# Optimization experiments

Hardware: AMD Instinct MI355X
Metric: run time of the kernel (lower is better)

Reference implementation:

```python
import jax, jax.numpy as jnp
import numpy as np

D = 256  # input_dim
B = 2048

def setup_inputs() -> dict:
    key = jax.random.key(0)
    ks = jax.random.split(key, 6)
    x = jax.random.normal(ks[0], (B, D), dtype=jnp.float32)
    offsets = jax.random.normal(ks[1], (D,), dtype=jnp.float32)
    coeff0 = jax.random.normal(ks[2], (), dtype=jnp.float32)
    coeff1 = jax.random.normal(ks[3], (D,), dtype=jnp.float32)
    coeff2 = jax.random.normal(ks[4], (D, D), dtype=jnp.float32)
    coeff3 = jax.random.normal(ks[5], (D, D, D), dtype=jnp.float32)
    return {"x": x, "offsets": offsets, "coeff0": coeff0, "coeff1": coeff1,
            "coeff2": coeff2, "coeff3": coeff3}

def reference(x, offsets, coeff0, coeff1, coeff2, coeff3):
    # Truncated Taylor series around learned offsets: out[b] = c0 + sum_i <coeff_i, rel^{\otimes i}>[b]
    rel = x - offsets  # (B, D)
    out = coeff0  # scalar, broadcasts to (B,)
    for c in (coeff1, coeff2, coeff3):
        # contract one mode of the rank-i coefficient with rel at a time
        t = jnp.einsum('...d,bd->b...', c, rel)  # (B, D^{i-1})
        while t.ndim > 1:
            t = jnp.einsum('b...d,bd->b...', t, rel)
        out = out + t  # (B,)
    return out
```

## Files before the change

### kernel.cpp

```cpp
#include <hip/hip_runtime.h>
#include <hip/hip_bf16.h>

#define DD 256
#define BB 2048
#define BM 128
#define BN 64
#define NTILE ((DD * DD) / BM)
#define NSTAGE (BB / BN)

typedef __bf16 bf16x8 __attribute__((ext_vector_type(8)));
typedef float  f32x4  __attribute__((ext_vector_type(4)));

#define AS1 __attribute__((address_space(1)))
#define AS3 __attribute__((address_space(3)))

__device__ __forceinline__ unsigned short f2bf(float f) {
    unsigned int u = __float_as_uint(f);
    return (unsigned short)((u + 0x7FFFu + ((u >> 16) & 1u)) >> 16);
}
__device__ __forceinline__ float bf2f(unsigned short s) {
    return __uint_as_float(((unsigned int)s) << 16);
}
__device__ __forceinline__ void async_cp16(const void* g, void* l) {
    __builtin_amdgcn_global_load_lds((const AS1 unsigned int*)g,
                                     (AS3 unsigned int*)l, 16, 0, 0);
}

__global__ void prep_all(const float* __restrict__ x, const float* __restrict__ offsets,
                         const float* __restrict__ c0, const float* __restrict__ c1,
                         float* __restrict__ rel_f32, unsigned short* __restrict__ rel_bf16,
                         float* __restrict__ out) {
    const int tid = threadIdx.x, wave = tid >> 6, lane = tid & 63;
    const float4 o4  = *(const float4*)(offsets + lane * 4);
    const float4 c14 = *(const float4*)(c1 + lane * 4);
#pragma unroll
    for (int i = 0; i < 2; ++i) {
        const int b = blockIdx.x * 8 + wave * 2 + i;
        const float4 x4 = *(const float4*)(x + (size_t)b * DD + lane * 4);
        float4 r;
        r.x = x4.x - o4.x; r.y = x4.y - o4.y; r.z = x4.z - o4.z; r.w = x4.w - o4.w;
        *(float4*)(rel_f32 + (size_t)b * DD + lane * 4) = r;
        ushort4 rb;
        rb.x = f2bf(r.x); rb.y = f2bf(r.y); rb.z = f2bf(r.z); rb.w = f2bf(r.w);
        *(ushort4*)(rel_bf16 + (size_t)b * DD + lane * 4) = rb;
        float s = r.x * c14.x + r.y * c14.y + r.z * c14.z + r.w * c14.w;
        s += __shfl_xor(s, 1);  s += __shfl_xor(s, 2);  s += __shfl_xor(s, 4);
        s += __shfl_xor(s, 8);  s += __shfl_xor(s, 16); s += __shfl_xor(s, 32);
        if (lane == 0) out[b] = c0[0] + s;
    }
}

__global__ __launch_bounds__(256, 2) void taylor3(
    const float* __restrict__ c3, const float* __restrict__ c2,
    const float* __restrict__ rel_f32, const unsigned short* __restrict__ rel_bf16,
    float* __restrict__ partial)
{
    __shared__ unsigned short Bs[2][BN * DD];
    __shared__ float relI[BB];
    __shared__ float c2row[BM];
    __shared__ float colsum[2][4][BN];

    const int tile = blockIdx.x;
    const int i_t   = tile >> 1;
    const int jbase = (tile & 1) << 7;
    const int tid  = threadIdx.x;
    const int wave = tid >> 6;
    const int lane = tid & 63;
    const int wm = wave & 1, wk = wave >> 1;
    const int lrow = lane & 15, quad = lane >> 4;

#pragma unroll
    for (int k = 0; k < 8; ++k) {
        const int b = tid + k * 256;
        relI[b] = rel_f32[(size_t)b * DD + i_t];
    }
    if (tid < BM) c2row[tid] = c2[i_t * DD + jbase + tid];

    bf16x8 afr[4][4];
    {
        const float* abase = c3 + (size_t)tile * BM * DD;
#pragma unroll
        for (int mt = 0; mt < 4; ++mt) {
            const int row = wm * 64 + mt * 16 + lrow;
            const float* p = abase + (size_t)row * DD + wk * 128 + quad * 8;
#pragma unroll
            for (int ks = 0; ks < 4; ++ks) {
                float4 f0 = *(const float4*)(p + ks * 32);
                float4 f1 = *(const float4*)(p + ks * 32 + 4);
                union { unsigned short u[8]; bf16x8 v; } cv;
                cv.u[0] = f2bf(f0.x); cv.u[1] = f2bf(f0.y);
                cv.u[2] = f2bf(f0.z); cv.u[3] = f2bf(f0.w);
                cv.u[4] = f2bf(f1.x); cv.u[5] = f2bf(f1.y);
                cv.u[6] = f2bf(f1.z); cv.u[7] = f2bf(f1.w);
                afr[ks][mt] = cv.v;
            }
        }
    }

    auto stage = [&](int nb, int buf) {
        const int b0 = nb * BN;
#pragma unroll
        for (int c = 0; c < 8; ++c) {
            const int r0 = c * 8 + wave * 2;
            const int row = r0 + (lane >> 5);
            const int g = (lane & 31) ^ (row & 7);
            const unsigned short* src = rel_bf16 + (size_t)(b0 + row) * DD + g * 8;
            async_cp16(src, &Bs[buf][r0 * DD]);
        }
    };

    stage(0, 0);
    int prev_b0 = -1;

    for (int nb = 0; nb < NSTAGE; ++nb) {
        const int cur = nb & 1;
        const int b0 = nb * BN;
        __syncthreads();
        if (nb + 1 < NSTAGE) stage(nb + 1, cur ^ 1);

        if (prev_b0 >= 0 && tid < BN) {
            const float v = colsum[cur ^ 1][0][tid] + colsum[cur ^ 1][1][tid]
                          + colsum[cur ^ 1][2][tid] + colsum[cur ^ 1][3][tid];
            partial[(size_t)tile * BB + prev_b0 + tid] = relI[prev_b0 + tid] * v;
        }

        f32x4 acc[4][4];
#pragma unroll
        for (int mt = 0; mt < 4; ++mt)
#pragma unroll
            for (int nt = 0; nt < 4; ++nt)
                acc[mt][nt] = (f32x4){0.f, 0.f, 0.f, 0.f};

#pragma unroll
        for (int ks = 0; ks < 4; ++ks) {
            const int glog = wk * 16 + ks * 4 + quad;
            bf16x8 bfr[4];
#pragma unroll
            for (int nt = 0; nt < 4; ++nt) {
                const int col = nt * 16 + lrow;
                const int g = glog ^ (col & 7);
                bfr[nt] = *(const bf16x8*)(&Bs[cur][col * DD + g * 8]);
            }
#pragma unroll
            for (int mt = 0; mt < 4; ++mt)
#pragma unroll
                for (int nt = 0; nt < 4; ++nt)
                    acc[mt][nt] = __builtin_amdgcn_mfma_f32_16x16x32_bf16(
                        afr[ks][mt], bfr[nt], acc[mt][nt], 0, 0, 0);
        }

        float sv[4];
#pragma unroll
        for (int nt = 0; nt < 4; ++nt) {
            const int col = nt * 16 + lrow;
            float s = 0.f;
#pragma unroll
            for (int mt = 0; mt < 4; ++mt) {
                const int el = wm * 64 + mt * 16 + quad * 4;
                const int e  = jbase + el;
                const int g  = (e >> 3) ^ (col & 7);
                const ushort4 rj = *(const ushort4*)(&Bs[cur][col * DD + g * 8 + (e & 7)]);
                float c2x = 0.f, c2y = 0.f, c2z = 0.f, c2w = 0.f;
                if (wk == 0) {
                    const float4 c2r = *(const float4*)(&c2row[el]);
                    c2x = c2r.x; c2y = c2r.y; c2z = c2r.z; c2w = c2r.w;
                }
                s += (acc[mt][nt][0] + c2x) * bf2f(rj.x);
                s += (acc[mt][nt][1] + c2y) * bf2f(rj.y);
                s += (acc[mt][nt][2] + c2z) * bf2f(rj.z);
                s += (acc[mt][nt][3] + c2w) * bf2f(rj.w);
            }
            s += __shfl_xor(s, 16, 64);
            s += __shfl_xor(s, 32, 64);
            sv[nt] = s;
        }
        {
            const float v01 = (quad & 1) ? sv[1] : sv[0];
            const float v23 = (quad & 1) ? sv[3] : sv[2];
            colsum[cur][wave][lane] = (quad & 2) ? v23 : v01;
        }
        prev_b0 = b0;
    }
    __syncthreads();
    if (tid < BN) {
        const float v = colsum[1][0][tid] + colsum[1][1][tid]
                      + colsum[1][2][tid] + colsum[1][3][tid];
        partial[(size_t)tile * BB + prev_b0 + tid] = relI[prev_b0 + tid] * v;
    }
}

__global__ void reduce_partial(const float* __restrict__ partial, float* __restrict__ out) {
    __shared__ f32x4 red[256];
    const int t = threadIdx.x;
    const int g = blockIdx.x * 4 + (t & 3);
    const int slice = t >> 2;
    f32x4 s = (f32x4){0.f, 0.f, 0.f, 0.f};
    for (int r = slice * 8; r < slice * 8 + 8; ++r)
        s += *(const f32x4*)(partial + (size_t)r * BB + g * 4);
    red[t] = s; __syncthreads();
    if (t < 128) red[t] += red[t + 128]; __syncthreads();
    if (t < 64)  red[t] += red[t + 64];  __syncthreads();
    if (t < 32)  red[t] += red[t + 32];  __syncthreads();
    if (t < 16)  red[t] += red[t + 16];  __syncthreads();
    if (t < 8)   red[t] += red[t + 8];   __syncthreads();
    if (t < 4) {
        const f32x4 v = red[t] + red[t + 4];
        float4* op = (float4*)(out + (size_t)(blockIdx.x * 4 + t) * 4);
        float4 o = *op;
        o.x += v[0]; o.y += v[1]; o.z += v[2]; o.w += v[3];
        *op = o;
    }
}

extern "C" void kernel_launch(void* const* d_in, const int* in_sizes, int n_in,
                              void* d_out, int out_size, void* d_ws, size_t ws_size,
                              hipStream_t stream) {
    const float* x       = (const float*)d_in[0];
    const float* offsets = (const float*)d_in[1];
    const float* c0      = (const float*)d_in[2];
    const float* c1      = (const float*)d_in[3];
    const float* c2      = (const float*)d_in[4];
    const float* c3      = (const float*)d_in[5];
    float* out = (float*)d_out;

    char* ws = (char*)d_ws;
    float* rel_f32 = (float*)ws;
    unsigned short* rel_bf16 = (unsigned short*)(ws + (size_t)BB * DD * 4);
    float* partial = (float*)(ws + (size_t)BB * DD * 6);

    prep_all<<<BB / 8, 256, 0, stream>>>(x, offsets, c0, c1, rel_f32, rel_bf16, out);
    taylor3<<<NTILE, 256, 0, stream>>>(c3, c2, rel_f32, rel_bf16, partial);
    reduce_partial<<<128, 256, 0, stream>>>(partial, out);
}
```

Measured before the change: 188.6 us.

## Split K dimension across blocks to double grid and raise occupancy

```diff
diff --git a/kernel.cpp b/kernel.cpp
--- a/kernel.cpp
+++ b/kernel.cpp
@@ -4,8 +4,8 @@
 #define DD 256
 #define BB 2048
 #define BM 128
-#define BN 64
-#define NTILE ((DD * DD) / BM)
+#define BN 32
+#define NBLK 1024
 #define NSTAGE (BB / BN)
 
 typedef __bf16 bf16x8 __attribute__((ext_vector_type(8)));
@@ -26,41 +26,32 @@
                                      (AS3 unsigned int*)l, 16, 0, 0);
 }
 
-__global__ void prep_all(const float* __restrict__ x, const float* __restrict__ offsets,
-                         const float* __restrict__ c0, const float* __restrict__ c1,
-                         float* __restrict__ rel_f32, unsigned short* __restrict__ rel_bf16,
-                         float* __restrict__ out) {
-    const int tid = threadIdx.x, wave = tid >> 6, lane = tid & 63;
-    const float4 o4  = *(const float4*)(offsets + lane * 4);
-    const float4 c14 = *(const float4*)(c1 + lane * 4);
-#pragma unroll
-    for (int i = 0; i < 2; ++i) {
-        const int b = blockIdx.x * 8 + wave * 2 + i;
-        const float4 x4 = *(const float4*)(x + (size_t)b * DD + lane * 4);
-        float4 r;
-        r.x = x4.x - o4.x; r.y = x4.y - o4.y; r.z = x4.z - o4.z; r.w = x4.w - o4.w;
-        *(float4*)(rel_f32 + (size_t)b * DD + lane * 4) = r;
-        ushort4 rb;
-        rb.x = f2bf(r.x); rb.y = f2bf(r.y); rb.z = f2bf(r.z); rb.w = f2bf(r.w);
-        *(ushort4*)(rel_bf16 + (size_t)b * DD + lane * 4) = rb;
-        float s = r.x * c14.x + r.y * c14.y + r.z * c14.z + r.w * c14.w;
-        s += __shfl_xor(s, 1);  s += __shfl_xor(s, 2);  s += __shfl_xor(s, 4);
-        s += __shfl_xor(s, 8);  s += __shfl_xor(s, 16); s += __shfl_xor(s, 32);
-        if (lane == 0) out[b] = c0[0] + s;
-    }
-}
-
-__global__ __launch_bounds__(256, 2) void taylor3(
+__global__ void prep_rel(const float* __restrict__ x, const float* __restrict__ offsets,
+                         float* __restrict__ rel_f32, unsigned short* __restrict__ rel_bf16) {
+    const int fi = blockIdx.x * 256 + threadIdx.x;
+    const int d4 = fi & 63;
+    const float4 o4 = ((const float4*)offsets)[d4];
+    const float4 x4 = ((const float4*)x)[fi];
+    float4 r;
+    r.x = x4.x - o4.x; r.y = x4.y - o4.y; r.z = x4.z - o4.z; r.w = x4.w - o4.w;
+    ((float4*)rel_f32)[fi] = r;
+    ushort4 rb;
+    rb.x = f2bf(r.x); rb.y = f2bf(r.y); rb.z = f2bf(r.z); rb.w = f2bf(r.w);
+    ((ushort4*)rel_bf16)[fi] = rb;
+}
+
+__global__ __launch_bounds__(256, 4) void taylor3(
     const float* __restrict__ c3, const float* __restrict__ c2,
     const float* __restrict__ rel_f32, const unsigned short* __restrict__ rel_bf16,
     float* __restrict__ partial)
 {
-    __shared__ unsigned short Bs[2][BN * DD];
-    __shared__ float relI[BB];
+    __shared__ unsigned short Bs[2][BN * 128];
     __shared__ float c2row[BM];
     __shared__ float colsum[2][4][BN];
 
-    const int tile = blockIdx.x;
+    const int bid  = blockIdx.x;
+    const int tile = bid >> 1;
+    const int kh   = bid & 1;
     const int i_t   = tile >> 1;
     const int jbase = (tile & 1) << 7;
     const int tid  = threadIdx.x;
@@ -69,22 +60,18 @@
     const int wm = wave & 1, wk = wave >> 1;
     const int lrow = lane & 15, quad = lane >> 4;
 
-#pragma unroll
-    for (int k = 0; k < 8; ++k) {
-        const int b = tid + k * 256;
-        relI[b] = rel_f32[(size_t)b * DD + i_t];
-    }
     if (tid < BM) c2row[tid] = c2[i_t * DD + jbase + tid];
 
-    bf16x8 afr[4][4];
+    bf16x8 afr[2][4];
     {
         const float* abase = c3 + (size_t)tile * BM * DD;
+        const int koff = kh * 128 + wk * 64 + quad * 8;
 #pragma unroll
         for (int mt = 0; mt < 4; ++mt) {
             const int row = wm * 64 + mt * 16 + lrow;
-            const float* p = abase + (size_t)row * DD + wk * 128 + quad * 8;
-#pragma unroll
-            for (int ks = 0; ks < 4; ++ks) {
+            const float* p = abase + (size_t)row * DD + koff;
+#pragma unroll
+            for (int ks = 0; ks < 2; ++ks) {
                 float4 f0 = *(const float4*)(p + ks * 32);
                 float4 f1 = *(const float4*)(p + ks * 32 + 4);
                 union { unsigned short u[8]; bf16x8 v; } cv;
@@ -100,12 +87,12 @@
     auto stage = [&](int nb, int buf) {
         const int b0 = nb * BN;
 #pragma unroll
-        for (int c = 0; c < 8; ++c) {
-            const int r0 = c * 8 + wave * 2;
-            const int row = r0 + (lane >> 5);
-            const int g = (lane & 31) ^ (row & 7);
-            const unsigned short* src = rel_bf16 + (size_t)(b0 + row) * DD + g * 8;
-            async_cp16(src, &Bs[buf][r0 * DD]);
+        for (int c = 0; c < 2; ++c) {
+            const int r0 = c * 16 + wave * 4;
+            const int row = r0 + (lane >> 4);
+            const int gsrc = (lane & 15) ^ (row & 15);
+            const unsigned short* src = rel_bf16 + (size_t)(b0 + row) * DD + kh * 128 + gsrc * 8;
+            async_cp16(src, &Bs[buf][r0 * 128]);
         }
     };
 
@@ -121,95 +108,107 @@
         if (prev_b0 >= 0 && tid < BN) {
             const float v = colsum[cur ^ 1][0][tid] + colsum[cur ^ 1][1][tid]
                           + colsum[cur ^ 1][2][tid] + colsum[cur ^ 1][3][tid];
-            partial[(size_t)tile * BB + prev_b0 + tid] = relI[prev_b0 + tid] * v;
-        }
-
-        f32x4 acc[4][4];
+            const float relI = rel_f32[(size_t)(prev_b0 + tid) * DD + i_t];
+            partial[(size_t)bid * BB + prev_b0 + tid] = relI * v;
+        }
+
+        ushort4 rj[2][4];
+#pragma unroll
+        for (int nt = 0; nt < 2; ++nt) {
+            const int bg = b0 + nt * 16 + lrow;
+#pragma unroll
+            for (int mt = 0; mt < 4; ++mt) {
+                const int e = jbase + wm * 64 + mt * 16 + quad * 4;
+                rj[nt][mt] = *(const ushort4*)(rel_bf16 + (size_t)bg * DD + e);
+            }
+        }
+
+        f32x4 acc[4][2];
 #pragma unroll
         for (int mt = 0; mt < 4; ++mt)
 #pragma unroll
-            for (int nt = 0; nt < 4; ++nt)
+            for (int nt = 0; nt < 2; ++nt)
                 acc[mt][nt] = (f32x4){0.f, 0.f, 0.f, 0.f};
 
 #pragma unroll
-        for (int ks = 0; ks < 4; ++ks) {
-            const int glog = wk * 16 + ks * 4 + quad;
-            bf16x8 bfr[4];
-#pragma unroll
-            for (int nt = 0; nt < 4; ++nt) {
+        for (int ks = 0; ks < 2; ++ks) {
+            const int glog = wk * 8 + ks * 4 + quad;
+            bf16x8 bfr[2];
+#pragma unroll
+            for (int nt = 0; nt < 2; ++nt) {
                 const int col = nt * 16 + lrow;
-                const int g = glog ^ (col & 7);
-                bfr[nt] = *(const bf16x8*)(&Bs[cur][col * DD + g * 8]);
+                const int g = glog ^ (col & 15);
+                bfr[nt] = *(const bf16x8*)(&Bs[cur][col * 128 + g * 8]);
             }
 #pragma unroll
             for (int mt = 0; mt < 4; ++mt)
 #pragma unroll
-                for (int nt = 0; nt < 4; ++nt)
+                for (int nt = 0; nt < 2; ++nt)
                     acc[mt][nt] = __builtin_amdgcn_mfma_f32_16x16x32_bf16(
                         afr[ks][mt], bfr[nt], acc[mt][nt], 0, 0, 0);
         }
 
-        float sv[4];
-#pragma unroll
-        for (int nt = 0; nt < 4; ++nt) {
-            const int col = nt * 16 + lrow;
+        const bool addc2 = (kh == 0) && (wk == 0);
+        float sv[2];
+#pragma unroll
+        for (int nt = 0; nt < 2; ++nt) {
             float s = 0.f;
 #pragma unroll
             for (int mt = 0; mt < 4; ++mt) {
                 const int el = wm * 64 + mt * 16 + quad * 4;
-                const int e  = jbase + el;
-                const int g  = (e >> 3) ^ (col & 7);
-                const ushort4 rj = *(const ushort4*)(&Bs[cur][col * DD + g * 8 + (e & 7)]);
                 float c2x = 0.f, c2y = 0.f, c2z = 0.f, c2w = 0.f;
-                if (wk == 0) {
+                if (addc2) {
                     const float4 c2r = *(const float4*)(&c2row[el]);
                     c2x = c2r.x; c2y = c2r.y; c2z = c2r.z; c2w = c2r.w;
                 }
-                s += (acc[mt][nt][0] + c2x) * bf2f(rj.x);
-                s += (acc[mt][nt][1] + c2y) * bf2f(rj.y);
-                s += (acc[mt][nt][2] + c2z) * bf2f(rj.z);
-                s += (acc[mt][nt][3] + c2w) * bf2f(rj.w);
+                const ushort4 r4 = rj[nt][mt];
+                s += (acc[mt][nt][0] + c2x) * bf2f(r4.x);
+                s += (acc[mt][nt][1] + c2y) * bf2f(r4.y);
+                s += (acc[mt][nt][2] + c2z) * bf2f(r4.z);
+                s += (acc[mt][nt][3] + c2w) * bf2f(r4.w);
             }
             s += __shfl_xor(s, 16, 64);
             s += __shfl_xor(s, 32, 64);
             sv[nt] = s;
         }
-        {
-            const float v01 = (quad & 1) ? sv[1] : sv[0];
-            const float v23 = (quad & 1) ? sv[3] : sv[2];
-            colsum[cur][wave][lane] = (quad & 2) ? v23 : v01;
-        }
+        if (lane < 32) colsum[cur][wave][lane] = (lane >> 4) ? sv[1] : sv[0];
         prev_b0 = b0;
     }
     __syncthreads();
     if (tid < BN) {
         const float v = colsum[1][0][tid] + colsum[1][1][tid]
                       + colsum[1][2][tid] + colsum[1][3][tid];
-        partial[(size_t)tile * BB + prev_b0 + tid] = relI[prev_b0 + tid] * v;
-    }
-}
-
-__global__ void reduce_partial(const float* __restrict__ partial, float* __restrict__ out) {
-    __shared__ f32x4 red[256];
+        const float relI = rel_f32[(size_t)(prev_b0 + tid) * DD + i_t];
+        partial[(size_t)bid * BB + prev_b0 + tid] = relI * v;
+    }
+}
+
+__global__ void reduce_partial(const float* __restrict__ partial,
+                               const float* __restrict__ rel_f32,
+                               const float* __restrict__ c0, const float* __restrict__ c1,
+                               float* __restrict__ out) {
+    __shared__ float red[256];
+    __shared__ float red2[256];
     const int t = threadIdx.x;
-    const int g = blockIdx.x * 4 + (t & 3);
-    const int slice = t >> 2;
-    f32x4 s = (f32x4){0.f, 0.f, 0.f, 0.f};
-    for (int r = slice * 8; r < slice * 8 + 8; ++r)
-        s += *(const f32x4*)(partial + (size_t)r * BB + g * 4);
-    red[t] = s; __syncthreads();
-    if (t < 128) red[t] += red[t + 128]; __syncthreads();
-    if (t < 64)  red[t] += red[t + 64];  __syncthreads();
-    if (t < 32)  red[t] += red[t + 32];  __syncthreads();
-    if (t < 16)  red[t] += red[t + 16];  __syncthreads();
-    if (t < 8)   red[t] += red[t + 8];   __syncthreads();
-    if (t < 4) {
-        const f32x4 v = red[t] + red[t + 4];
-        float4* op = (float4*)(out + (size_t)(blockIdx.x * 4 + t) * 4);
-        float4 o = *op;
-        o.x += v[0]; o.y += v[1]; o.z += v[2]; o.w += v[3];
-        *op = o;
-    }
+    const int bl = t & 15;
+    const int slice = t >> 4;
+    const int bbase = blockIdx.x * 16;
+    float s = 0.f;
+    for (int i = 0; i < 64; ++i)
+        s += partial[(size_t)(slice * 64 + i) * BB + bbase + bl];
+    red[t] = s;
+    float d = 0.f;
+#pragma unroll
+    for (int e = 0; e < 16; ++e) {
+        const int k = slice * 16 + e;
+        d += c1[k] * rel_f32[(size_t)(bbase + bl) * DD + k];
+    }
+    red2[t] = d;
+    __syncthreads();
+    if (t < 128) { red[t] += red[t + 128]; red2[t] += red2[t + 128]; } __syncthreads();
+    if (t < 64)  { red[t] += red[t + 64];  red2[t] += red2[t + 64];  } __syncthreads();
+    if (t < 32)  { red[t] += red[t + 32];  red2[t] += red2[t + 32];  } __syncthreads();
+    if (t < 16)  out[bbase + t] = c0[0] + red[t] + red[t + 16] + red2[t] + red2[t + 16];
 }
 
 extern "C" void kernel_launch(void* const* d_in, const int* in_sizes, int n_in,
@@ -228,7 +227,7 @@
     unsigned short* rel_bf16 = (unsigned short*)(ws + (size_t)BB * DD * 4);
     float* partial = (float*)(ws + (size_t)BB * DD * 6);
 
-    prep_all<<<BB / 8, 256, 0, stream>>>(x, offsets, c0, c1, rel_f32, rel_bf16, out);
-    taylor3<<<NTILE, 256, 0, stream>>>(c3, c2, rel_f32, rel_bf16, partial);
-    reduce_partial<<<128, 256, 0, stream>>>(partial, out);
-}
+    prep_rel<<<512, 256, 0, stream>>>(x, offsets, rel_f32, rel_bf16);
+    taylor3<<<NBLK, 256, 0, stream>>>(c3, c2, rel_f32, rel_bf16, partial);
+    reduce_partial<<<128, 256, 0, stream>>>(partial, rel_f32, c0, c1, out);
+}
```

After: 386.9 us. 105% more time.
